# Kernel tuning notes

Measured on AMD Instinct MI355X. Metric: run time of the kernel, lower is better.

Reference implementation:

```python
import jax, jax.numpy as jnp
import numpy as np

N, E, H, NH = 10000, 160000, 128, 8
HD = H // NH
LDIM = 8  # (lmax+1)**2 - 1 with lmax=2
CUTOFF = 5.0


def setup_inputs() -> dict:
    key = jax.random.key(0)
    ks = jax.random.split(key, 20)
    w = lambda k, shape: jax.random.normal(k, shape, jnp.float32) * 0.05
    return dict(
        node_feats=jax.random.normal(ks[0], (N, H), jnp.float32),
        edge_feats=jax.random.normal(ks[1], (E, H), jnp.float32),
        vector_feats=jax.random.normal(ks[2], (N, LDIM, H), jnp.float32),
        distances=jax.random.uniform(ks[3], (E,), jnp.float32) * CUTOFF,
        d_ij=jax.random.normal(ks[4], (E, LDIM), jnp.float32),
        senders=jax.random.randint(ks[5], (E,), 0, N),
        receivers=jax.random.randint(ks[6], (E,), 0, N),
        ln_scale=jnp.ones((H,), jnp.float32),
        ln_bias=jnp.zeros((H,), jnp.float32),
        vln_w=jnp.ones((H,), jnp.float32),
        W_vec=w(ks[7], (H, 3 * H)),
        Wq=w(ks[8], (H, H)), bq=jnp.zeros((H,), jnp.float32),
        Wk=w(ks[9], (H, H)), bk=jnp.zeros((H,), jnp.float32),
        Wv=w(ks[10], (H, H)), bv=jnp.zeros((H,), jnp.float32),
        Wdk=w(ks[11], (H, H)), bdk=jnp.zeros((H,), jnp.float32),
        Wdv=w(ks[12], (H, H)), bdv=jnp.zeros((H,), jnp.float32),
        Ws=w(ks[13], (H, 2 * H)), bs=jnp.zeros((2 * H,), jnp.float32),
        Wo=w(ks[14], (H, 3 * H)), bo=jnp.zeros((3 * H,), jnp.float32),
        Wf=w(ks[15], (H, H)), bf=jnp.zeros((H,), jnp.float32),
        Wsrc=w(ks[16], (H, H)),
        Wtrg=w(ks[17], (H, H)),
    )


def _reject(vec, d):
    # vector rejection of vec [E, L, H] against direction d [E, L]
    proj = (vec * d[:, :, None]).sum(axis=1, keepdims=True)
    return vec - proj * d[:, :, None]


def _forward(node_feats, edge_feats, vector_feats, distances, d_ij, senders, receivers,
             ln_scale, ln_bias, vln_w, W_vec, Wq, bq, Wk, bk, Wv, bv, Wdk, bdk, Wdv, bdv,
             Ws, bs, Wo, bo, Wf, bf, Wsrc, Wtrg):
    silu = jax.nn.silu
    n = node_feats.shape[0]
    # LayerNorm (eps=1e-5) on node feats
    mu = node_feats.mean(-1, keepdims=True)
    xc = node_feats - mu
    var = (xc * xc).mean(-1, keepdims=True)
    x = xc * jax.lax.rsqrt(var + 1e-5) * ln_scale + ln_bias
    # VecLayerNorm with norm_type='none' -> identity norm + learned per-channel scale
    vec = vector_feats * vln_w
    q = (x @ Wq + bq).reshape(-1, NH, HD)
    k = (x @ Wk + bk).reshape(-1, NH, HD)
    v = (x @ Wv + bv).reshape(-1, NH, HD)
    dk = silu(edge_feats @ Wdk + bdk).reshape(-1, NH, HD)
    dv = silu(edge_feats @ Wdv + bdv).reshape(-1, NH, HD)
    vec1, vec2, vec3 = jnp.split(vec @ W_vec, [H, 2 * H], axis=-1)
    vec_dot = (vec1 * vec2).sum(axis=1)  # [N, H]
    # per-edge gathers
    q_i = q[receivers]
    k_j = k[senders]
    v_j = v[senders]
    vec_j = vec[senders]  # [E, LDIM, H]
    # attention-style message with cosine cutoff
    cut = 0.5 * (jnp.cos(distances * (jnp.pi / CUTOFF)) + 1.0) * (distances < CUTOFF)
    attn = silu((q_i * k_j * dk).sum(-1)) * cut[:, None]  # [E, NH]
    vj = ((v_j * dv) * attn[:, :, None]).reshape(-1, H)   # [E, H]
    s1, s2 = jnp.split(silu(vj @ Ws + bs), [H], axis=1)
    vec_msg = vec_j * s1[:, None, :] + s2[:, None, :] * d_ij[:, :, None]
    # scatter reduce to nodes
    node_agg = jax.ops.segment_sum(vj, receivers, num_segments=n)
    vec_agg = jax.ops.segment_sum(vec_msg, receivers, num_segments=n)
    o1, o2, o3 = jnp.split(node_agg @ Wo + bo, [H, 2 * H], axis=1)
    dx = vec_dot * o2 + o3
    dvec = vec3 * o1[:, None, :] + vec_agg
    # edge update (last_layer=False)
    w1 = _reject(vec[receivers] @ Wtrg, d_ij)
    w2 = _reject(vec_j @ Wsrc, -d_ij)
    w_dot = (w1 * w2).sum(axis=1)  # [E, H]
    df_ij = silu(edge_feats @ Wf + bf) * w_dot
    return dx, df_ij, dvec


def reference(node_feats, edge_feats, vector_feats, distances, d_ij, senders, receivers,
              ln_scale, ln_bias, vln_w, W_vec, Wq, bq, Wk, bk, Wv, bv, Wdk, bdk, Wdv, bdv,
              Ws, bs, Wo, bo, Wf, bf, Wsrc, Wtrg):
    return _forward(node_feats, edge_feats, vector_feats, distances, d_ij, senders, receivers,
                    ln_scale, ln_bias, vln_w, W_vec, Wq, bq, Wk, bk, Wv, bv, Wdk, bdk, Wdv, bdv,
                    Ws, bs, Wo, bo, Wf, bf, Wsrc, Wtrg)
```

## Files before the change

kernel.cpp:

```cpp
#include <hip/hip_runtime.h>
#include <math.h>

#define NN 10000
#define NE 160000
#define H  128
#define LD 8

typedef unsigned short ushort_t;
typedef short bf16x8 __attribute__((ext_vector_type(8)));
typedef float f32x4 __attribute__((ext_vector_type(4)));

__device__ __forceinline__ float silu_f(float x){ return x / (1.0f + expf(-x)); }
__device__ __forceinline__ float4 f4z(){ return make_float4(0.f,0.f,0.f,0.f); }

__device__ __forceinline__ ushort_t f2bf(float f){
    union { float f; unsigned int u; } x; x.f = f;
    unsigned int r = x.u + 0x7FFFu + ((x.u >> 16) & 1u);
    return (ushort_t)(r >> 16);
}
__device__ __forceinline__ unsigned int pack2bf(float a, float b){
    return (unsigned int)f2bf(a) | ((unsigned int)f2bf(b) << 16);
}
__device__ __forceinline__ float bf2f_hi(unsigned int u){
    union { unsigned int u; float f; } x; x.u = u & 0xffff0000u; return x.f;
}
__device__ __forceinline__ float bf2f_lo(unsigned int u){
    union { unsigned int u; float f; } x; x.u = u << 16; return x.f;
}
__device__ __forceinline__ float bfu2f(ushort_t u){
    union { unsigned int u; float f; } x; x.u = ((unsigned int)u) << 16; return x.f;
}

__global__ void k_prepw(const float* __restrict__ Wq, const float* __restrict__ Wk,
                        const float* __restrict__ Wv, const float* __restrict__ W_vec,
                        const float* __restrict__ Wtrg, const float* __restrict__ Wsrc,
                        const float* __restrict__ Wdk, const float* __restrict__ Wdv,
                        const float* __restrict__ Ws,  const float* __restrict__ Wf,
                        ushort_t* __restrict__ wqkvT, ushort_t* __restrict__ wvecT,
                        ushort_t* __restrict__ wdkT, ushort_t* __restrict__ wdvT,
                        ushort_t* __restrict__ wsT,
                        ushort_t* __restrict__ wfT_hi, ushort_t* __restrict__ wfT_lo){
    int i = blockIdx.x * 256 + threadIdx.x;
    int n = i >> 7, kk = i & 127;
    if (n < 384){
        float v;
        if (n < 128)      v = Wq[kk*128 + n];
        else if (n < 256) v = Wk[kk*128 + (n-128)];
        else              v = Wv[kk*128 + (n-256)];
        wqkvT[n*128 + kk] = f2bf(v);
    } else if (n < 1024){
        int m = n - 384;
        float v;
        if (m < 384)      v = W_vec[kk*384 + m];
        else if (m < 512) v = Wtrg[kk*128 + (m-384)];
        else              v = Wsrc[kk*128 + (m-512)];
        wvecT[m*128 + kk] = f2bf(v);
    } else if (n < 1152){
        int m = n - 1024;
        wdkT[m*128 + kk] = f2bf(Wdk[kk*128 + m]);
    } else if (n < 1280){
        int m = n - 1152;
        wdvT[m*128 + kk] = f2bf(Wdv[kk*128 + m]);
    } else if (n < 1536){
        int m = n - 1280;
        wsT[m*128 + kk] = f2bf(Ws[kk*256 + m]);
    } else if (n < 1664){
        int m = n - 1536;
        float v = Wf[kk*128 + m];
        ushort_t hi = f2bf(v);
        wfT_hi[m*128 + kk] = hi;
        wfT_lo[m*128 + kk] = f2bf(v - bfu2f(hi));
    }
}

__global__ void k_hist(const int* __restrict__ rcv, int* __restrict__ cnt){
    int e = blockIdx.x * 256 + threadIdx.x;
    if (e < NE) atomicAdd(&cnt[rcv[e]], 1);
}

__global__ __launch_bounds__(256) void k_scan(const int* __restrict__ cnt, int* __restrict__ offs){
    __shared__ int part[256];
    const int t = threadIdx.x;
    const int CH = 40;
    int loc[CH];
    int base = t * CH;
    int lsum = 0;
    if (base < NN){
        #pragma unroll
        for (int i = 0; i < CH; i++){ loc[i] = cnt[base + i]; lsum += loc[i]; }
    }
    part[t] = lsum;
    __syncthreads();
    for (int off = 1; off < 256; off <<= 1){
        int v = (t >= off) ? part[t - off] : 0;
        __syncthreads();
        part[t] += v;
        __syncthreads();
    }
    int ex = part[t] - lsum;
    if (base < NN){
        int run = ex;
        #pragma unroll
        for (int i = 0; i < CH; i++){ offs[base + i] = run; run += loc[i]; }
    }
    if (t == 255) offs[NN] = part[255];
}

__global__ void k_scatter(const int* __restrict__ rcv, const int* __restrict__ offs,
                          int* __restrict__ cnt2, int* __restrict__ eidx){
    int e = blockIdx.x * 256 + threadIdx.x;
    if (e < NE){
        int r = rcv[e];
        int p = atomicAdd(&cnt2[r], 1);
        eidx[offs[r] + p] = e;
    }
}

__global__ __launch_bounds__(256) void k_perm(
    const float* __restrict__ ef, const int* __restrict__ eidx,
    const int* __restrict__ snd, const int* __restrict__ rcv,
    const float* __restrict__ dist, const float* __restrict__ dij,
    float* __restrict__ ef_srt, ushort_t* __restrict__ ef_bf_srt,
    int* __restrict__ snd_srt, int* __restrict__ rcv_srt,
    float* __restrict__ dist_srt, float* __restrict__ dij_srt)
{
    __shared__ int eidx_s[64];
    const int tid = threadIdx.x;
    const int p0  = blockIdx.x * 64;
    if (tid < 64){
        int p = p0 + tid;
        int e = eidx[p];
        eidx_s[tid] = e;
        snd_srt[p]  = snd[e];
        rcv_srt[p]  = rcv[e];
        dist_srt[p] = dist[e];
    }
    __syncthreads();
    const int r = tid >> 2, cq = tid & 3;
    const int e = eidx_s[r];
    const int p = p0 + r;
    const float4* src = (const float4*)(ef + (size_t)e*H + cq*32);
    float4* dst  = (float4*)(ef_srt + (size_t)p*H + cq*32);
    ushort_t* db = ef_bf_srt + (size_t)p*H + cq*32;
    #pragma unroll
    for (int j = 0; j < 8; j++){
        float4 v = src[j];
        dst[j] = v;
        uint2 u; u.x = pack2bf(v.x, v.y); u.y = pack2bf(v.z, v.w);
        *(uint2*)(db + j*4) = u;
    }
    if (cq == 0){
        *(float4*)(dij_srt + (size_t)p*LD)     = *(const float4*)(dij + (size_t)e*LD);
        *(float4*)(dij_srt + (size_t)p*LD + 4) = *(const float4*)(dij + (size_t)e*LD + 4);
    }
}

__global__ __launch_bounds__(128) void node_ln(
    const float* __restrict__ nf, const float* __restrict__ vf,
    const float* __restrict__ ln_s, const float* __restrict__ ln_b,
    const float* __restrict__ vlnw,
    ushort_t* __restrict__ x_bf, ushort_t* __restrict__ vec_bf,
    ushort_t* __restrict__ vec_t)
{
    const int n = blockIdx.x, h = threadIdx.x;
    __shared__ float red[4];
    float xv = nf[(size_t)n*H + h];
    float s1 = xv, s2 = xv*xv;
    #pragma unroll
    for (int o = 32; o >= 1; o >>= 1){
        s1 += __shfl_xor(s1, o, 64);
        s2 += __shfl_xor(s2, o, 64);
    }
    const int wid = h >> 6;
    if ((h & 63) == 0){ red[wid] = s1; red[2+wid] = s2; }
    __syncthreads();
    float mean = (red[0] + red[1]) * (1.0f/H);
    float var  = (red[2] + red[3]) * (1.0f/H) - mean*mean;
    float x = (xv - mean) * rsqrtf(var + 1e-5f) * ln_s[h] + ln_b[h];
    x_bf[(size_t)n*H + h] = f2bf(x);
    float w = vlnw[h];
    union { ushort_t s[8]; uint4 u; } pk;
    #pragma unroll
    for (int l = 0; l < LD; l++){
        size_t i = ((size_t)n*LD + l)*H + h;
        ushort_t b = f2bf(vf[i] * w);
        vec_bf[i] = b;
        pk.s[l] = b;
    }
    *(uint4*)&vec_t[((size_t)n*H + h)*8] = pk.u;
}

__global__ __launch_bounds__(256) void node_qkv(
    const ushort_t* __restrict__ x_bf, const ushort_t* __restrict__ wqkvT,
    const float* __restrict__ bq, const float* __restrict__ bk, const float* __restrict__ bv,
    float* __restrict__ q, ushort_t* __restrict__ k_bf, ushort_t* __restrict__ v_bf)
{
    const int tid  = threadIdx.x;
    const int lane = tid & 63;
    const int m0   = (tid >> 6) * 16;
    const int e0   = blockIdx.x * 64;

    const int mrow = lane & 15;
    const int kblk = lane >> 4;

    f32x4 acc[24];
    #pragma unroll
    for (int nt = 0; nt < 24; nt++) acc[nt] = (f32x4)(0.f);

    int arow = e0 + m0 + mrow; if (arow >= NN) arow = NN-1;
    const ushort_t* Arow = x_bf + (size_t)arow*H + kblk*8;
    const ushort_t* wb   = wqkvT + (size_t)mrow*H + kblk*8;

    #pragma unroll
    for (int ks = 0; ks < 4; ks++){
        bf16x8 a = *(const bf16x8*)(Arow + ks*32);
        #pragma unroll
        for (int nt = 0; nt < 24; nt++){
            bf16x8 b8 = *(const bf16x8*)(wb + (size_t)nt*16*H + ks*32);
            acc[nt] = __builtin_amdgcn_mfma_f32_16x16x32_bf16(a, b8, acc[nt], 0, 0, 0);
        }
    }
    #pragma unroll
    for (int t = 0; t < 8; t++){
        int col = t*16 + mrow;
        float bb = bq[col];
        #pragma unroll
        for (int r = 0; r < 4; r++){
            int row = e0 + m0 + kblk*4 + r;
            if (row < NN) q[(size_t)row*H + col] = acc[t][r] + bb;
        }
    }
    #pragma unroll
    for (int t = 0; t < 8; t++){
        int col = t*16 + mrow;
        float bb = bk[col];
        #pragma unroll
        for (int r = 0; r < 4; r++){
            int row = e0 + m0 + kblk*4 + r;
            if (row < NN) k_bf[(size_t)row*H + col] = f2bf(acc[8+t][r] + bb);
        }
    }
    #pragma unroll
    for (int t = 0; t < 8; t++){
        int col = t*16 + mrow;
        float bb = bv[col];
        #pragma unroll
        for (int r = 0; r < 4; r++){
            int row = e0 + m0 + kblk*4 + r;
            if (row < NN) v_bf[(size_t)row*H + col] = f2bf(acc[16+t][r] + bb);
        }
    }
}

__global__ __launch_bounds__(256) void node_vec(
    const ushort_t* __restrict__ vec_bf, const ushort_t* __restrict__ wvecT,
    float* __restrict__ vdot, ushort_t* __restrict__ vec3,
    ushort_t* __restrict__ Vt_t, ushort_t* __restrict__ Vs_t)
{
    __shared__ ushort_t st_s[64][136];

    const int tid  = threadIdx.x;
    const int lane = tid & 63;
    const int wv   = tid >> 6;
    const int m0   = wv * 16;
    const size_t r0 = (size_t)blockIdx.x * 64;

    const int mrow = lane & 15;
    const int kblk = lane >> 4;

    f32x4 acc[40];
    #pragma unroll
    for (int nt = 0; nt < 40; nt++) acc[nt] = (f32x4)(0.f);

    const ushort_t* Arow = vec_bf + (r0 + m0 + mrow)*H + kblk*8;
    const ushort_t* wb   = wvecT + (size_t)mrow*H + kblk*8;

    #pragma unroll
    for (int ks = 0; ks < 4; ks++){
        bf16x8 a = *(const bf16x8*)(Arow + ks*32);
        #pragma unroll
        for (int nt = 0; nt < 40; nt++){
            bf16x8 b8 = *(const bf16x8*)(wb + (size_t)nt*16*H + ks*32);
            acc[nt] = __builtin_amdgcn_mfma_f32_16x16x32_bf16(a, b8, acc[nt], 0, 0, 0);
        }
    }

    #pragma unroll
    for (int t = 0; t < 8; t++){
        float p = acc[t][0]*acc[t+8][0] + acc[t][1]*acc[t+8][1]
                + acc[t][2]*acc[t+8][2] + acc[t][3]*acc[t+8][3];
        p += __shfl_xor(p, 16, 64);
        if ((kblk & 1) == 0){
            int node = (int)(r0 >> 3) + wv*2 + (kblk >> 1);
            vdot[(size_t)node*H + t*16 + mrow] = p;
        }
    }

    __syncthreads();
    #pragma unroll
    for (int t = 0; t < 8; t++){
        int coln = t*16 + mrow;
        int lr = m0 + kblk*4;
        st_s[lr+0][coln] = f2bf(acc[16+t][0]);
        st_s[lr+1][coln] = f2bf(acc[16+t][1]);
        st_s[lr+2][coln] = f2bf(acc[16+t][2]);
        st_s[lr+3][coln] = f2bf(acc[16+t][3]);
    }
    __syncthreads();
    {
        const int rr = tid >> 2, qq = tid & 3;
        uint4* dst = (uint4*)&vec3[(r0 + rr)*H + qq*32];
        const uint4* src = (const uint4*)&st_s[rr][qq*32];
        dst[0] = src[0]; dst[1] = src[1]; dst[2] = src[2]; dst[3] = src[3];
    }

    #pragma unroll
    for (int g = 0; g < 2; g++){
        __syncthreads();
        const int base = 24 + g*8;
        #pragma unroll
        for (int t = 0; t < 8; t++){
            int coln = t*16 + mrow;
            int lr = m0 + kblk*4;
            st_s[lr+0][coln] = f2bf(acc[base+t][0]);
            st_s[lr+1][coln] = f2bf(acc[base+t][1]);
            st_s[lr+2][coln] = f2bf(acc[base+t][2]);
            st_s[lr+3][coln] = f2bf(acc[base+t][3]);
        }
        __syncthreads();
        ushort_t* dstb = (g == 0) ? Vt_t : Vs_t;
        #pragma unroll
        for (int j = 0; j < 4; j++){
            int p = tid + 256*j;
            int nl = p >> 7, hh = p & 127;
            union { ushort_t s[8]; uint4 u; } pk;
            #pragma unroll
            for (int l = 0; l < 8; l++) pk.s[l] = st_s[nl*8 + l][hh];
            *(uint4*)&dstb[(((r0 >> 3) + nl)*(size_t)H + hh)*8] = pk.u;
        }
    }
}

__global__ __launch_bounds__(256) void edge_attn(
    const ushort_t* __restrict__ ef_bf,
    const ushort_t* __restrict__ wdkT, const float* __restrict__ bdk,
    const ushort_t* __restrict__ wdvT, const float* __restrict__ bdv,
    const int* __restrict__ snd_srt, const int* __restrict__ rcv_srt,
    const float* __restrict__ dist_srt,
    const float* __restrict__ q, const ushort_t* __restrict__ k_bf,
    const ushort_t* __restrict__ v_bf,
    ushort_t* __restrict__ vj)
{
    __shared__ ushort_t dk_s[64][136];
    __shared__ ushort_t dv_s[64][136];

    const int tid  = threadIdx.x;
    const int lane = tid & 63;
    const int m0   = (tid >> 6) * 16;
    const size_t e0 = (size_t)blockIdx.x * 64;

    const int mrow = lane & 15;
    const int kblk = lane >> 4;

    f32x4 accK[8], accV[8];
    #pragma unroll
    for (int nt = 0; nt < 8; nt++){ accK[nt] = (f32x4)(0.f); accV[nt] = (f32x4)(0.f); }

    const ushort_t* Arow = ef_bf + (e0 + m0 + mrow)*H + kblk*8;
    const ushort_t* wkb  = wdkT + (size_t)mrow*H + kblk*8;
    const ushort_t* wvb  = wdvT + (size_t)mrow*H + kblk*8;

    #pragma unroll
    for (int ks = 0; ks < 4; ks++){
        bf16x8 a = *(const bf16x8*)(Arow + ks*32);
        #pragma unroll
        for (int nt = 0; nt < 8; nt++){
            bf16x8 bk8 = *(const bf16x8*)(wkb + (size_t)nt*16*H + ks*32);
            accK[nt] = __builtin_amdgcn_mfma_f32_16x16x32_bf16(a, bk8, accK[nt], 0, 0, 0);
            bf16x8 bv8 = *(const bf16x8*)(wvb + (size_t)nt*16*H + ks*32);
            accV[nt] = __builtin_amdgcn_mfma_f32_16x16x32_bf16(a, bv8, accV[nt], 0, 0, 0);
        }
    }

    const int lrow = m0 + 4*kblk;
    #pragma unroll
    for (int nt = 0; nt < 8; nt++){
        int coln = nt*16 + mrow;
        float bkn = bdk[coln], bvn = bdv[coln];
        #pragma unroll
        for (int r = 0; r < 4; r++){
            dk_s[lrow + r][coln] = f2bf(silu_f(accK[nt][r] + bkn));
            dv_s[lrow + r][coln] = f2bf(silu_f(accV[nt][r] + bvn));
        }
    }
    __syncthreads();

    const int r  = tid >> 2, cq = tid & 3;
    const size_t e = e0 + r;
    const int s  = snd_srt[e], rr = rcv_srt[e];
    const float d = dist_srt[e];
    const float cut = (d < 5.0f) ? 0.5f*(cosf(d*0.6283185307179586f) + 1.0f) : 0.0f;
    const float*    qrow = q    + (size_t)rr*H + cq*32;
    const ushort_t* krow = k_bf + (size_t)s*H + cq*32;
    const ushort_t* vrow = v_bf + (size_t)s*H + cq*32;
    ushort_t* vjrow = vj + e*H + cq*32;

    #pragma unroll
    for (int hh = 0; hh < 2; hh++){
        const int c0 = hh*16;
        float p = 0.f;
        #pragma unroll
        for (int j = 0; j < 4; j++){
            float4 q4 = *(const float4*)(qrow + c0 + 4*j);
            uint2 ku = *(const uint2*)(krow + c0 + 4*j);
            uint2 du = *(const uint2*)&dk_s[r][cq*32 + c0 + 4*j];
            p += q4.x*bf2f_lo(ku.x)*bf2f_lo(du.x) + q4.y*bf2f_hi(ku.x)*bf2f_hi(du.x)
               + q4.z*bf2f_lo(ku.y)*bf2f_lo(du.y) + q4.w*bf2f_hi(ku.y)*bf2f_hi(du.y);
        }
        float attn = silu_f(p) * cut;
        #pragma unroll
        for (int j = 0; j < 4; j++){
            uint2 vu = *(const uint2*)(vrow + c0 + 4*j);
            uint2 du = *(const uint2*)&dv_s[r][cq*32 + c0 + 4*j];
            uint2 u;
            u.x = pack2bf(bf2f_lo(vu.x)*bf2f_lo(du.x)*attn,
                          bf2f_hi(vu.x)*bf2f_hi(du.x)*attn);
            u.y = pack2bf(bf2f_lo(vu.y)*bf2f_lo(du.y)*attn,
                          bf2f_hi(vu.y)*bf2f_hi(du.y)*attn);
            *(uint2*)(vjrow + c0 + 4*j) = u;
        }
    }
}

__global__ __launch_bounds__(256) void edge_s(
    const ushort_t* __restrict__ vj, const ushort_t* __restrict__ wsT,
    const float* __restrict__ bs, unsigned int* __restrict__ s12p)
{
    __shared__ ushort_t s_s[64][264];

    const int tid  = threadIdx.x;
    const int lane = tid & 63;
    const int m0   = (tid >> 6) * 16;
    const size_t e0 = (size_t)blockIdx.x * 64;

    const int mrow = lane & 15;
    const int kblk = lane >> 4;

    f32x4 acc[16];
    #pragma unroll
    for (int nt = 0; nt < 16; nt++) acc[nt] = (f32x4)(0.f);

    const ushort_t* Arow = vj + (e0 + m0 + mrow)*H + kblk*8;
    const ushort_t* wb   = wsT + (size_t)mrow*H + kblk*8;

    #pragma unroll
    for (int ks = 0; ks < 4; ks++){
        bf16x8 a = *(const bf16x8*)(Arow + ks*32);
        #pragma unroll
        for (int nt = 0; nt < 16; nt++){
            bf16x8 b8 = *(const bf16x8*)(wb + (size_t)nt*16*H + ks*32);
            acc[nt] = __builtin_amdgcn_mfma_f32_16x16x32_bf16(a, b8, acc[nt], 0, 0, 0);
        }
    }

    const int lrow = m0 + 4*kblk;
    #pragma unroll
    for (int nt = 0; nt < 16; nt++){
        int coln = nt*16 + mrow;
        float bb = bs[coln];
        #pragma unroll
        for (int r = 0; r < 4; r++)
            s_s[lrow + r][coln] = f2bf(silu_f(acc[nt][r] + bb));
    }
    __syncthreads();

    const int r = tid >> 2, cq = tid & 3;
    #pragma unroll
    for (int j = 0; j < 8; j++){
        int hh = cq*32 + j*4;
        uint4 o;
        o.x = (unsigned)s_s[r][hh+0] | ((unsigned)s_s[r][128+hh+0] << 16);
        o.y = (unsigned)s_s[r][hh+1] | ((unsigned)s_s[r][128+hh+1] << 16);
        o.z = (unsigned)s_s[r][hh+2] | ((unsigned)s_s[r][128+hh+2] << 16);
        o.w = (unsigned)s_s[r][hh+3] | ((unsigned)s_s[r][128+hh+3] << 16);
        *(uint4*)&s12p[(e0 + r)*H + hh] = o;
    }
}

__global__ __launch_bounds__(256) void edge_f(
    const float* __restrict__ ef,
    const ushort_t* __restrict__ wfT_hi, const ushort_t* __restrict__ wfT_lo,
    const float* __restrict__ bf_, float* __restrict__ f)
{
    const int tid  = threadIdx.x;
    const int lane = tid & 63;
    const int m0   = (tid >> 6) * 16;
    const size_t e0 = (size_t)blockIdx.x * 64;

    const int mrow = lane & 15;
    const int kblk = lane >> 4;

    f32x4 acc[8];
    #pragma unroll
    for (int nt = 0; nt < 8; nt++) acc[nt] = (f32x4)(0.f);

    const float* Arow = ef + (e0 + m0 + mrow)*H + kblk*8;
    const ushort_t* wh = wfT_hi + (size_t)mrow*H + kblk*8;
    const ushort_t* wl = wfT_lo + (size_t)mrow*H + kblk*8;

    #pragma unroll
    for (int ks = 0; ks < 4; ks++){
        float4 v0 = *(const float4*)(Arow + ks*32);
        float4 v1 = *(const float4*)(Arow + ks*32 + 4);
        float vv[8] = {v0.x, v0.y, v0.z, v0.w, v1.x, v1.y, v1.z, v1.w};
        union { short s[8]; bf16x8 v; } ah, al;
        #pragma unroll
        for (int j = 0; j < 8; j++){
            ushort_t hi = f2bf(vv[j]);
            ah.s[j] = (short)hi;
            al.s[j] = (short)f2bf(vv[j] - bfu2f(hi));
        }
        #pragma unroll
        for (int nt = 0; nt < 8; nt++){
            bf16x8 bh = *(const bf16x8*)(wh + (size_t)nt*16*H + ks*32);
            bf16x8 bl = *(const bf16x8*)(wl + (size_t)nt*16*H + ks*32);
            acc[nt] = __builtin_amdgcn_mfma_f32_16x16x32_bf16(ah.v, bh, acc[nt], 0, 0, 0);
            acc[nt] = __builtin_amdgcn_mfma_f32_16x16x32_bf16(al.v, bh, acc[nt], 0, 0, 0);
            acc[nt] = __builtin_amdgcn_mfma_f32_16x16x32_bf16(ah.v, bl, acc[nt], 0, 0, 0);
            acc[nt] = __builtin_amdgcn_mfma_f32_16x16x32_bf16(al.v, bl, acc[nt], 0, 0, 0);
        }
    }

    #pragma unroll
    for (int nt = 0; nt < 8; nt++){
        int col = nt*16 + mrow;
        float bb = bf_[col];
        #pragma unroll
        for (int r = 0; r < 4; r++)
            f[(e0 + m0 + 4*kblk + r)*H + col] = silu_f(acc[nt][r] + bb);
    }
}

struct Pref {
    int   s, eo;
    float vjv;
    unsigned p12;
    uint4 uv, ub;
    float4 d0, d1;
    float fv;
};

__global__ __launch_bounds__(512) void node_fuse(
    const int* __restrict__ offs, const int* __restrict__ eidx,
    const int* __restrict__ snd_srt,
    const ushort_t* __restrict__ vj, const unsigned int* __restrict__ s12p,
    const float* __restrict__ dij_srt, const ushort_t* __restrict__ vec_t,
    const float* __restrict__ f,
    const ushort_t* __restrict__ Vt_t, const ushort_t* __restrict__ Vs_t,
    const float* __restrict__ Wo, const float* __restrict__ bo,
    const float* __restrict__ vdot, const ushort_t* __restrict__ vec3,
    float* __restrict__ dx, float* __restrict__ df, float* __restrict__ dvec)
{
    const int n = blockIdx.x;
    const int tid = threadIdx.x;
    const int h = tid & 127;
    const int par = tid >> 7;
    const int beg = offs[n], end = offs[n+1];

    float AT[LD];
    {
        uint4 ut = *(const uint4*)&Vt_t[((size_t)n*H + h)*8];
        AT[0]=bf2f_lo(ut.x); AT[1]=bf2f_hi(ut.x);
        AT[2]=bf2f_lo(ut.y); AT[3]=bf2f_hi(ut.y);
        AT[4]=bf2f_lo(ut.z); AT[5]=bf2f_hi(ut.z);
        AT[6]=bf2f_lo(ut.w); AT[7]=bf2f_hi(ut.w);
    }

    float na = 0.f;
    float av[LD];
    #pragma unroll
    for (int l = 0; l < LD; l++) av[l] = 0.f;

    Pref cur, nxt;
    int i = beg + par;
    if (i < end){
        int s = snd_srt[i];
        cur.s   = s;
        cur.eo  = eidx[i];
        cur.vjv = bfu2f(vj[(size_t)i*H + h]);
        cur.p12 = s12p[(size_t)i*H + h];
        cur.uv  = *(const uint4*)&vec_t[((size_t)s*H + h)*8];
        cur.ub  = *(const uint4*)&Vs_t[((size_t)s*H + h)*8];
        cur.d0  = *(const float4*)&dij_srt[(size_t)i*LD];
        cur.d1  = *(const float4*)&dij_srt[(size_t)i*LD + 4];
        cur.fv  = f[(size_t)i*H + h];
    }

    while (i < end){
        const int j = i + 4;
        if (j < end){
            int s = snd_srt[j];
            nxt.s   = s;
            nxt.eo  = eidx[j];
            nxt.vjv = bfu2f(vj[(size_t)j*H + h]);
            nxt.p12 = s12p[(size_t)j*H + h];
            nxt.uv  = *(const uint4*)&vec_t[((size_t)s*H + h)*8];
            nxt.ub  = *(const uint4*)&Vs_t[((size_t)s*H + h)*8];
            nxt.d0  = *(const float4*)&dij_srt[(size_t)j*LD];
            nxt.d1  = *(const float4*)&dij_srt[(size_t)j*LD + 4];
            nxt.fv  = f[(size_t)j*H + h];
        }

        float s1 = bf2f_lo(cur.p12), s2 = bf2f_hi(cur.p12);
        na += cur.vjv;
        float dl[LD];
        dl[0]=cur.d0.x; dl[1]=cur.d0.y; dl[2]=cur.d0.z; dl[3]=cur.d0.w;
        dl[4]=cur.d1.x; dl[5]=cur.d1.y; dl[6]=cur.d1.z; dl[7]=cur.d1.w;
        float dd = 0.f;
        #pragma unroll
        for (int l = 0; l < LD; l++) dd = fmaf(dl[l], dl[l], dd);
        const float c2 = 2.0f - dd;

        float vvx[LD], Blx[LD];
        vvx[0]=bf2f_lo(cur.uv.x); vvx[1]=bf2f_hi(cur.uv.x);
        vvx[2]=bf2f_lo(cur.uv.y); vvx[3]=bf2f_hi(cur.uv.y);
        vvx[4]=bf2f_lo(cur.uv.z); vvx[5]=bf2f_hi(cur.uv.z);
        vvx[6]=bf2f_lo(cur.uv.w); vvx[7]=bf2f_hi(cur.uv.w);
        Blx[0]=bf2f_lo(cur.ub.x); Blx[1]=bf2f_hi(cur.ub.x);
        Blx[2]=bf2f_lo(cur.ub.y); Blx[3]=bf2f_hi(cur.ub.y);
        Blx[4]=bf2f_lo(cur.ub.z); Blx[5]=bf2f_hi(cur.ub.z);
        Blx[6]=bf2f_lo(cur.ub.w); Blx[7]=bf2f_hi(cur.ub.w);

        float AB = 0.f, aa_ = 0.f, bb_ = 0.f;
        #pragma unroll
        for (int l = 0; l < LD; l++){
            av[l] = fmaf(vvx[l], s1, fmaf(dl[l], s2, av[l]));
            AB  = fmaf(AT[l], Blx[l], AB);
            aa_ = fmaf(AT[l], dl[l], aa_);
            bb_ = fmaf(Blx[l], dl[l], bb_);
        }
        df[(size_t)cur.eo*H + h] = cur.fv * (AB - aa_*bb_*c2);

        cur = nxt;
        i = j;
    }

    __shared__ float pl[4][LD+1][128];
    __shared__ float o_s[3][128];
    #pragma unroll
    for (int l = 0; l < LD; l++) pl[par][l][h] = av[l];
    pl[par][LD][h] = na;
    __syncthreads();

    if (par == 0){
        #pragma unroll
        for (int l = 0; l <= LD; l++)
            pl[0][l][h] = (pl[0][l][h] + pl[1][l][h]) + (pl[2][l][h] + pl[3][l][h]);
    }
    __syncthreads();

    if (par > 0){
        const int g = par - 1;
        float o = bo[g*H + h];
        for (int kk = 0; kk < H; kk++)
            o = fmaf(pl[0][LD][kk], Wo[kk*(3*H) + g*H + h], o);
        o_s[g][h] = o;
    }
    __syncthreads();

    if (par == 0){
        dx[(size_t)n*H + h] = fmaf(vdot[(size_t)n*H + h], o_s[1][h], o_s[2][h]);
        #pragma unroll
        for (int l = 0; l < LD; l++){
            size_t i2 = ((size_t)n*LD + l)*H + h;
            dvec[i2] = fmaf(bfu2f(vec3[i2]), o_s[0][h], pl[0][l][h]);
        }
    }
}

extern "C" void kernel_launch(void* const* d_in, const int* in_sizes, int n_in,
                              void* d_out, int out_size, void* d_ws, size_t ws_size,
                              hipStream_t stream) {
    const float* nf    = (const float*)d_in[0];
    const float* ef    = (const float*)d_in[1];
    const float* vf    = (const float*)d_in[2];
    const float* dist  = (const float*)d_in[3];
    const float* dij   = (const float*)d_in[4];
    const int*   snd   = (const int*)d_in[5];
    const int*   rcv   = (const int*)d_in[6];
    const float* ln_s  = (const float*)d_in[7];
    const float* ln_b  = (const float*)d_in[8];
    const float* vlnw  = (const float*)d_in[9];
    const float* W_vec = (const float*)d_in[10];
    const float* Wq    = (const float*)d_in[11];
    const float* bq    = (const float*)d_in[12];
    const float* Wk    = (const float*)d_in[13];
    const float* bk    = (const float*)d_in[14];
    const float* Wv    = (const float*)d_in[15];
    const float* bv    = (const float*)d_in[16];
    const float* Wdk   = (const float*)d_in[17];
    const float* bdk   = (const float*)d_in[18];
    const float* Wdv   = (const float*)d_in[19];
    const float* bdv   = (const float*)d_in[20];
    const float* Ws    = (const float*)d_in[21];
    const float* bs    = (const float*)d_in[22];
    const float* Wo    = (const float*)d_in[23];
    const float* bo    = (const float*)d_in[24];
    const float* Wf    = (const float*)d_in[25];
    const float* bf_   = (const float*)d_in[26];
    const float* Wsrc  = (const float*)d_in[27];
    const float* Wtrg  = (const float*)d_in[28];

    float* out  = (float*)d_out;
    float* dx   = out;
    float* df   = out + (size_t)NN*H;
    float* dvec = df + (size_t)NE*H;

    float* w = (float*)d_ws;
    size_t off = 0;
    float* q    = w + off; off += (size_t)NN*H;
    float* vdot = w + off; off += (size_t)NN*H;
    ushort_t* k_bf   = (ushort_t*)(w + off); off += (size_t)NN*H/2;
    ushort_t* v_bf   = (ushort_t*)(w + off); off += (size_t)NN*H/2;
    ushort_t* x_bf   = (ushort_t*)(w + off); off += (size_t)NN*H/2;
    ushort_t* vec_bf = (ushort_t*)(w + off); off += (size_t)NN*LD*H/2;
    ushort_t* vec_t  = (ushort_t*)(w + off); off += (size_t)NN*LD*H/2;
    ushort_t* vec3   = (ushort_t*)(w + off); off += (size_t)NN*LD*H/2;
    ushort_t* Vt_t   = (ushort_t*)(w + off); off += (size_t)NN*LD*H/2;
    ushort_t* Vs_t   = (ushort_t*)(w + off); off += (size_t)NN*LD*H/2;
    ushort_t* vj     = (ushort_t*)(w + off); off += (size_t)NE*H/2;
    float*        ef_srt = (float*)(w + off);
    unsigned int* s12p   = (unsigned int*)(w + off); off += (size_t)NE*H;
    ushort_t* ef_bf_srt = (ushort_t*)(w + off);
    float*    f         = (float*)(w + off); off += (size_t)NE*H;
    ushort_t* wqkvT  = (ushort_t*)(w + off); off += 384*128/2;
    ushort_t* wvecT  = (ushort_t*)(w + off); off += 640*128/2;
    ushort_t* wdkT   = (ushort_t*)(w + off); off += 128*128/2;
    ushort_t* wdvT   = (ushort_t*)(w + off); off += 128*128/2;
    ushort_t* wsT    = (ushort_t*)(w + off); off += 256*128/2;
    ushort_t* wfT_hi = (ushort_t*)(w + off); off += 128*128/2;
    ushort_t* wfT_lo = (ushort_t*)(w + off); off += 128*128/2;
    int* cnt  = (int*)(w + off); off += NN;
    int* cnt2 = (int*)(w + off); off += NN;
    int* offs = (int*)(w + off); off += NN + 1;
    int* eidx = (int*)(w + off); off += NE;
    int* snd_srt = (int*)(w + off); off += NE;
    int* rcv_srt = (int*)(w + off); off += NE;
    float* dist_srt = (float*)(w + off); off += NE;
    float* dij_srt  = (float*)(w + off); off += (size_t)NE*LD;

    hipMemsetAsync(cnt,  0, NN*sizeof(int), stream);
    hipMemsetAsync(cnt2, 0, NN*sizeof(int), stream);

    k_prepw<<<832, 256, 0, stream>>>(Wq, Wk, Wv, W_vec, Wtrg, Wsrc, Wdk, Wdv, Ws, Wf,
                                     wqkvT, wvecT, wdkT, wdvT, wsT, wfT_hi, wfT_lo);

    k_hist<<<(NE+255)/256, 256, 0, stream>>>(rcv, cnt);
    k_scan<<<1, 256, 0, stream>>>(cnt, offs);
    k_scatter<<<(NE+255)/256, 256, 0, stream>>>(rcv, offs, cnt2, eidx);

    k_perm<<<NE/64, 256, 0, stream>>>(ef, eidx, snd, rcv, dist, dij,
                                      ef_srt, ef_bf_srt, snd_srt, rcv_srt,
                                      dist_srt, dij_srt);

    node_ln<<<NN, 128, 0, stream>>>(nf, vf, ln_s, ln_b, vlnw, x_bf, vec_bf, vec_t);

    node_qkv<<<(NN+63)/64, 256, 0, stream>>>(x_bf, wqkvT, bq, bk, bv, q, k_bf, v_bf);

    node_vec<<<NN*LD/64, 256, 0, stream>>>(vec_bf, wvecT, vdot, vec3, Vt_t, Vs_t);

    edge_attn<<<NE/64, 256, 0, stream>>>(ef_bf_srt, wdkT, bdk, wdvT, bdv,
                                         snd_srt, rcv_srt, dist_srt, q, k_bf, v_bf, vj);

    edge_f<<<NE/64, 256, 0, stream>>>(ef_srt, wfT_hi, wfT_lo, bf_, f);

    edge_s<<<NE/64, 256, 0, stream>>>(vj, wsT, bs, s12p);

    node_fuse<<<NN, 512, 0, stream>>>(offs, eidx, snd_srt, vj, s12p, dij_srt, vec_t,
                                      f, Vt_t, Vs_t, Wo, bo, vdot, vec3, dx, df, dvec);
}
```

Measured before the change: 883.3 us.

## Fuse edge attention, Wf and Ws GEMMs into one edge kernel with bf16 intermediates

Merges edge_attn, edge_f and edge_s into a single per-64-edge kernel. vj is kept in shared memory for the Ws GEMM rather than re-read from global. k_perm now writes precomputed hi/lo bf16 splits of the edge features instead of an fp32 copy plus a bf16 copy, and the silu(ef@Wf) result is stored as bf16 in place over the lo buffer rather than as fp32. This cuts global traffic and launch count, at the cost of higher register and shared-memory pressure per block and reduced precision of f in the df output.

New measurement: 893.0 us. Within noise of the previous version (+1.1%).

```diff
diff --git a/kernel.cpp b/kernel.cpp
--- a/kernel.cpp
+++ b/kernel.cpp
@@ -11,7 +11,6 @@
 typedef float f32x4 __attribute__((ext_vector_type(4)));
 
 __device__ __forceinline__ float silu_f(float x){ return x / (1.0f + expf(-x)); }
-__device__ __forceinline__ float4 f4z(){ return make_float4(0.f,0.f,0.f,0.f); }
 
 __device__ __forceinline__ ushort_t f2bf(float f){
     union { float f; unsigned int u; } x; x.f = f;
@@ -120,7 +119,7 @@
     const float* __restrict__ ef, const int* __restrict__ eidx,
     const int* __restrict__ snd, const int* __restrict__ rcv,
     const float* __restrict__ dist, const float* __restrict__ dij,
-    float* __restrict__ ef_srt, ushort_t* __restrict__ ef_bf_srt,
+    ushort_t* __restrict__ ef_hi, ushort_t* __restrict__ ef_lo,
     int* __restrict__ snd_srt, int* __restrict__ rcv_srt,
     float* __restrict__ dist_srt, float* __restrict__ dij_srt)
 {
@@ -140,14 +139,19 @@
     const int e = eidx_s[r];
     const int p = p0 + r;
     const float4* src = (const float4*)(ef + (size_t)e*H + cq*32);
-    float4* dst  = (float4*)(ef_srt + (size_t)p*H + cq*32);
-    ushort_t* db = ef_bf_srt + (size_t)p*H + cq*32;
+    ushort_t* dh = ef_hi + (size_t)p*H + cq*32;
+    ushort_t* dl = ef_lo + (size_t)p*H + cq*32;
     #pragma unroll
     for (int j = 0; j < 8; j++){
         float4 v = src[j];
-        dst[j] = v;
-        uint2 u; u.x = pack2bf(v.x, v.y); u.y = pack2bf(v.z, v.w);
-        *(uint2*)(db + j*4) = u;
+        ushort_t hx = f2bf(v.x), hy = f2bf(v.y), hz = f2bf(v.z), hw = f2bf(v.w);
+        ushort_t lx = f2bf(v.x - bfu2f(hx)), ly = f2bf(v.y - bfu2f(hy));
+        ushort_t lz = f2bf(v.z - bfu2f(hz)), lw = f2bf(v.w - bfu2f(hw));
+        uint2 uh, ul;
+        uh.x = (unsigned)hx | ((unsigned)hy << 16); uh.y = (unsigned)hz | ((unsigned)hw << 16);
+        ul.x = (unsigned)lx | ((unsigned)ly << 16); ul.y = (unsigned)lz | ((unsigned)lw << 16);
+        *(uint2*)(dh + j*4) = uh;
+        *(uint2*)(dl + j*4) = ul;
     }
     if (cq == 0){
         *(float4*)(dij_srt + (size_t)p*LD)     = *(const float4*)(dij + (size_t)e*LD);
@@ -341,203 +345,176 @@
     }
 }
 
-__global__ __launch_bounds__(256) void edge_attn(
-    const ushort_t* __restrict__ ef_bf,
+__global__ __launch_bounds__(256) void edge_mega(
+    const ushort_t* __restrict__ ef_hi, ushort_t* __restrict__ ef_lo_f,
     const ushort_t* __restrict__ wdkT, const float* __restrict__ bdk,
     const ushort_t* __restrict__ wdvT, const float* __restrict__ bdv,
+    const ushort_t* __restrict__ wfT_hi, const ushort_t* __restrict__ wfT_lo,
+    const float* __restrict__ bf_,
+    const ushort_t* __restrict__ wsT, const float* __restrict__ bs,
     const int* __restrict__ snd_srt, const int* __restrict__ rcv_srt,
     const float* __restrict__ dist_srt,
     const float* __restrict__ q, const ushort_t* __restrict__ k_bf,
     const ushort_t* __restrict__ v_bf,
-    ushort_t* __restrict__ vj)
+    ushort_t* __restrict__ vj, unsigned int* __restrict__ s12p)
 {
-    __shared__ ushort_t dk_s[64][136];
-    __shared__ ushort_t dv_s[64][136];
+    __shared__ union {
+        struct { ushort_t dk[64][136]; ushort_t dv[64][136]; } a;
+        ushort_t s_s[64][264];
+    } U;
+    __shared__ ushort_t vj_s[64][136];
 
     const int tid  = threadIdx.x;
     const int lane = tid & 63;
     const int m0   = (tid >> 6) * 16;
     const size_t e0 = (size_t)blockIdx.x * 64;
-
     const int mrow = lane & 15;
     const int kblk = lane >> 4;
 
-    f32x4 accK[8], accV[8];
-    #pragma unroll
-    for (int nt = 0; nt < 8; nt++){ accK[nt] = (f32x4)(0.f); accV[nt] = (f32x4)(0.f); }
-
-    const ushort_t* Arow = ef_bf + (e0 + m0 + mrow)*H + kblk*8;
-    const ushort_t* wkb  = wdkT + (size_t)mrow*H + kblk*8;
-    const ushort_t* wvb  = wdvT + (size_t)mrow*H + kblk*8;
-
-    #pragma unroll
-    for (int ks = 0; ks < 4; ks++){
-        bf16x8 a = *(const bf16x8*)(Arow + ks*32);
+    {
+        f32x4 accK[8], accV[8];
+        #pragma unroll
+        for (int nt = 0; nt < 8; nt++){ accK[nt] = (f32x4)(0.f); accV[nt] = (f32x4)(0.f); }
+        const ushort_t* Arow = ef_hi + (e0 + m0 + mrow)*H + kblk*8;
+        const ushort_t* wkb  = wdkT + (size_t)mrow*H + kblk*8;
+        const ushort_t* wvb  = wdvT + (size_t)mrow*H + kblk*8;
+        #pragma unroll
+        for (int ks = 0; ks < 4; ks++){
+            bf16x8 a = *(const bf16x8*)(Arow + ks*32);
+            #pragma unroll
+            for (int nt = 0; nt < 8; nt++){
+                bf16x8 bk8 = *(const bf16x8*)(wkb + (size_t)nt*16*H + ks*32);
+                accK[nt] = __builtin_amdgcn_mfma_f32_16x16x32_bf16(a, bk8, accK[nt], 0, 0, 0);
+                bf16x8 bv8 = *(const bf16x8*)(wvb + (size_t)nt*16*H + ks*32);
+                accV[nt] = __builtin_amdgcn_mfma_f32_16x16x32_bf16(a, bv8, accV[nt], 0, 0, 0);
+            }
+        }
+        const int lrow = m0 + 4*kblk;
         #pragma unroll
         for (int nt = 0; nt < 8; nt++){
-            bf16x8 bk8 = *(const bf16x8*)(wkb + (size_t)nt*16*H + ks*32);
-            accK[nt] = __builtin_amdgcn_mfma_f32_16x16x32_bf16(a, bk8, accK[nt], 0, 0, 0);
-            bf16x8 bv8 = *(const bf16x8*)(wvb + (size_t)nt*16*H + ks*32);
-            accV[nt] = __builtin_amdgcn_mfma_f32_16x16x32_bf16(a, bv8, accV[nt], 0, 0, 0);
-        }
-    }
-
-    const int lrow = m0 + 4*kblk;
-    #pragma unroll
-    for (int nt = 0; nt < 8; nt++){
-        int coln = nt*16 + mrow;
-        float bkn = bdk[coln], bvn = bdv[coln];
-        #pragma unroll
-        for (int r = 0; r < 4; r++){
-            dk_s[lrow + r][coln] = f2bf(silu_f(accK[nt][r] + bkn));
-            dv_s[lrow + r][coln] = f2bf(silu_f(accV[nt][r] + bvn));
-        }
-    }
-    __syncthreads();
-
-    const int r  = tid >> 2, cq = tid & 3;
-    const size_t e = e0 + r;
-    const int s  = snd_srt[e], rr = rcv_srt[e];
-    const float d = dist_srt[e];
-    const float cut = (d < 5.0f) ? 0.5f*(cosf(d*0.6283185307179586f) + 1.0f) : 0.0f;
-    const float*    qrow = q    + (size_t)rr*H + cq*32;
-    const ushort_t* krow = k_bf + (size_t)s*H + cq*32;
-    const ushort_t* vrow = v_bf + (size_t)s*H + cq*32;
-    ushort_t* vjrow = vj + e*H + cq*32;
-
-    #pragma unroll
-    for (int hh = 0; hh < 2; hh++){
-        const int c0 = hh*16;
-        float p = 0.f;
-        #pragma unroll
-        for (int j = 0; j < 4; j++){
-            float4 q4 = *(const float4*)(qrow + c0 + 4*j);
-            uint2 ku = *(const uint2*)(krow + c0 + 4*j);
-            uint2 du = *(const uint2*)&dk_s[r][cq*32 + c0 + 4*j];
-            p += q4.x*bf2f_lo(ku.x)*bf2f_lo(du.x) + q4.y*bf2f_hi(ku.x)*bf2f_hi(du.x)
-               + q4.z*bf2f_lo(ku.y)*bf2f_lo(du.y) + q4.w*bf2f_hi(ku.y)*bf2f_hi(du.y);
-        }
-        float attn = silu_f(p) * cut;
-        #pragma unroll
-        for (int j = 0; j < 4; j++){
-            uint2 vu = *(const uint2*)(vrow + c0 + 4*j);
-            uint2 du = *(const uint2*)&dv_s[r][cq*32 + c0 + 4*j];
-            uint2 u;
-            u.x = pack2bf(bf2f_lo(vu.x)*bf2f_lo(du.x)*attn,
-                          bf2f_hi(vu.x)*bf2f_hi(du.x)*attn);
-            u.y = pack2bf(bf2f_lo(vu.y)*bf2f_lo(du.y)*attn,
-                          bf2f_hi(vu.y)*bf2f_hi(du.y)*attn);
-            *(uint2*)(vjrow + c0 + 4*j) = u;
-        }
-    }
-}
-
-__global__ __launch_bounds__(256) void edge_s(
-    const ushort_t* __restrict__ vj, const ushort_t* __restrict__ wsT,
-    const float* __restrict__ bs, unsigned int* __restrict__ s12p)
-{
-    __shared__ ushort_t s_s[64][264];
-
-    const int tid  = threadIdx.x;
-    const int lane = tid & 63;
-    const int m0   = (tid >> 6) * 16;
-    const size_t e0 = (size_t)blockIdx.x * 64;
-
-    const int mrow = lane & 15;
-    const int kblk = lane >> 4;
-
-    f32x4 acc[16];
-    #pragma unroll
-    for (int nt = 0; nt < 16; nt++) acc[nt] = (f32x4)(0.f);
-
-    const ushort_t* Arow = vj + (e0 + m0 + mrow)*H + kblk*8;
-    const ushort_t* wb   = wsT + (size_t)mrow*H + kblk*8;
-
-    #pragma unroll
-    for (int ks = 0; ks < 4; ks++){
-        bf16x8 a = *(const bf16x8*)(Arow + ks*32);
+            int coln = nt*16 + mrow;
+            float bkn = bdk[coln], bvn = bdv[coln];
+            #pragma unroll
+            for (int r = 0; r < 4; r++){
+                U.a.dk[lrow + r][coln] = f2bf(silu_f(accK[nt][r] + bkn));
+                U.a.dv[lrow + r][coln] = f2bf(silu_f(accV[nt][r] + bvn));
+            }
+        }
+    }
+    __syncthreads();
+
+    {
+        const int r  = tid >> 2, cq = tid & 3;
+        const size_t e = e0 + r;
+        const int s  = snd_srt[e], rr = rcv_srt[e];
+        const float d = dist_srt[e];
+        const float cut = (d < 5.0f) ? 0.5f*(cosf(d*0.6283185307179586f) + 1.0f) : 0.0f;
+        const float*    qrow = q    + (size_t)rr*H + cq*32;
+        const ushort_t* krow = k_bf + (size_t)s*H + cq*32;
+        const ushort_t* vrow = v_bf + (size_t)s*H + cq*32;
+        ushort_t* vjrow = vj + e*H + cq*32;
+
+        #pragma unroll
+        for (int hh = 0; hh < 2; hh++){
+            const int c0 = hh*16;
+            float p = 0.f;
+            #pragma unroll
+            for (int j = 0; j < 4; j++){
+                float4 q4 = *(const float4*)(qrow + c0 + 4*j);
+                uint2 ku = *(const uint2*)(krow + c0 + 4*j);
+                uint2 du = *(const uint2*)&U.a.dk[r][cq*32 + c0 + 4*j];
+                p += q4.x*bf2f_lo(ku.x)*bf2f_lo(du.x) + q4.y*bf2f_hi(ku.x)*bf2f_hi(du.x)
+                   + q4.z*bf2f_lo(ku.y)*bf2f_lo(du.y) + q4.w*bf2f_hi(ku.y)*bf2f_hi(du.y);
+            }
+            float attn = silu_f(p) * cut;
+            #pragma unroll
+            for (int j = 0; j < 4; j++){
+                uint2 vu = *(const uint2*)(vrow + c0 + 4*j);
+                uint2 du = *(const uint2*)&U.a.dv[r][cq*32 + c0 + 4*j];
+                uint2 u;
+                u.x = pack2bf(bf2f_lo(vu.x)*bf2f_lo(du.x)*attn,
+                              bf2f_hi(vu.x)*bf2f_hi(du.x)*attn);
+                u.y = pack2bf(bf2f_lo(vu.y)*bf2f_lo(du.y)*attn,
+                              bf2f_hi(vu.y)*bf2f_hi(du.y)*attn);
+                *(uint2*)(vjrow + c0 + 4*j) = u;
+                *(uint2*)&vj_s[r][cq*32 + c0 + 4*j] = u;
+            }
+        }
+    }
+    __syncthreads();
+
+    {
+        f32x4 accF[8];
+        #pragma unroll
+        for (int nt = 0; nt < 8; nt++) accF[nt] = (f32x4)(0.f);
+        const ushort_t* Ah = ef_hi   + (e0 + m0 + mrow)*H + kblk*8;
+        const ushort_t* Al = ef_lo_f + (e0 + m0 + mrow)*H + kblk*8;
+        const ushort_t* wh = wfT_hi + (size_t)mrow*H + kblk*8;
+        const ushort_t* wl = wfT_lo + (size_t)mrow*H + kblk*8;
+        #pragma unroll
+        for (int ks = 0; ks < 4; ks++){
+            bf16x8 ah = *(const bf16x8*)(Ah + ks*32);
+            bf16x8 al = *(const bf16x8*)(Al + ks*32);
+            #pragma unroll
+            for (int nt = 0; nt < 8; nt++){
+                bf16x8 bh = *(const bf16x8*)(wh + (size_t)nt*16*H + ks*32);
+                bf16x8 bl = *(const bf16x8*)(wl + (size_t)nt*16*H + ks*32);
+                accF[nt] = __builtin_amdgcn_mfma_f32_16x16x32_bf16(ah, bh, accF[nt], 0, 0, 0);
+                accF[nt] = __builtin_amdgcn_mfma_f32_16x16x32_bf16(al, bh, accF[nt], 0, 0, 0);
+                accF[nt] = __builtin_amdgcn_mfma_f32_16x16x32_bf16(ah, bl, accF[nt], 0, 0, 0);
+                accF[nt] = __builtin_amdgcn_mfma_f32_16x16x32_bf16(al, bl, accF[nt], 0, 0, 0);
+            }
+        }
+        __syncthreads();
+        #pragma unroll
+        for (int nt = 0; nt < 8; nt++){
+            int col = nt*16 + mrow;
+            float bb = bf_[col];
+            #pragma unroll
+            for (int r = 0; r < 4; r++)
+                ef_lo_f[(e0 + m0 + 4*kblk + r)*H + col] = f2bf(silu_f(accF[nt][r] + bb));
+        }
+    }
+
+    {
+        f32x4 accS[16];
+        #pragma unroll
+        for (int nt = 0; nt < 16; nt++) accS[nt] = (f32x4)(0.f);
+        const ushort_t* ArowL = &vj_s[m0 + mrow][kblk*8];
+        const ushort_t* wb    = wsT + (size_t)mrow*H + kblk*8;
+        #pragma unroll
+        for (int ks = 0; ks < 4; ks++){
+            bf16x8 a = *(const bf16x8*)(ArowL + ks*32);
+            #pragma unroll
+            for (int nt = 0; nt < 16; nt++){
+                bf16x8 b8 = *(const bf16x8*)(wb + (size_t)nt*16*H + ks*32);
+                accS[nt] = __builtin_amdgcn_mfma_f32_16x16x32_bf16(a, b8, accS[nt], 0, 0, 0);
+            }
+        }
+        const int lrow = m0 + 4*kblk;
         #pragma unroll
         for (int nt = 0; nt < 16; nt++){
-            bf16x8 b8 = *(const bf16x8*)(wb + (size_t)nt*16*H + ks*32);
-            acc[nt] = __builtin_amdgcn_mfma_f32_16x16x32_bf16(a, b8, acc[nt], 0, 0, 0);
-        }
-    }
-
-    const int lrow = m0 + 4*kblk;
-    #pragma unroll
-    for (int nt = 0; nt < 16; nt++){
-        int coln = nt*16 + mrow;
-        float bb = bs[coln];
-        #pragma unroll
-        for (int r = 0; r < 4; r++)
-            s_s[lrow + r][coln] = f2bf(silu_f(acc[nt][r] + bb));
-    }
-    __syncthreads();
-
-    const int r = tid >> 2, cq = tid & 3;
-    #pragma unroll
-    for (int j = 0; j < 8; j++){
-        int hh = cq*32 + j*4;
-        uint4 o;
-        o.x = (unsigned)s_s[r][hh+0] | ((unsigned)s_s[r][128+hh+0] << 16);
-        o.y = (unsigned)s_s[r][hh+1] | ((unsigned)s_s[r][128+hh+1] << 16);
-        o.z = (unsigned)s_s[r][hh+2] | ((unsigned)s_s[r][128+hh+2] << 16);
-        o.w = (unsigned)s_s[r][hh+3] | ((unsigned)s_s[r][128+hh+3] << 16);
-        *(uint4*)&s12p[(e0 + r)*H + hh] = o;
-    }
-}
-
-__global__ __launch_bounds__(256) void edge_f(
-    const float* __restrict__ ef,
-    const ushort_t* __restrict__ wfT_hi, const ushort_t* __restrict__ wfT_lo,
-    const float* __restrict__ bf_, float* __restrict__ f)
-{
-    const int tid  = threadIdx.x;
-    const int lane = tid & 63;
-    const int m0   = (tid >> 6) * 16;
-    const size_t e0 = (size_t)blockIdx.x * 64;
-
-    const int mrow = lane & 15;
-    const int kblk = lane >> 4;
-
-    f32x4 acc[8];
-    #pragma unroll
-    for (int nt = 0; nt < 8; nt++) acc[nt] = (f32x4)(0.f);
-
-    const float* Arow = ef + (e0 + m0 + mrow)*H + kblk*8;
-    const ushort_t* wh = wfT_hi + (size_t)mrow*H + kblk*8;
-    const ushort_t* wl = wfT_lo + (size_t)mrow*H + kblk*8;
-
-    #pragma unroll
-    for (int ks = 0; ks < 4; ks++){
-        float4 v0 = *(const float4*)(Arow + ks*32);
-        float4 v1 = *(const float4*)(Arow + ks*32 + 4);
-        float vv[8] = {v0.x, v0.y, v0.z, v0.w, v1.x, v1.y, v1.z, v1.w};
-        union { short s[8]; bf16x8 v; } ah, al;
+            int coln = nt*16 + mrow;
+            float bb = bs[coln];
+            #pragma unroll
+            for (int r = 0; r < 4; r++)
+                U.s_s[lrow + r][coln] = f2bf(silu_f(accS[nt][r] + bb));
+        }
+    }
+    __syncthreads();
+
+    {
+        const int r = tid >> 2, cq = tid & 3;
         #pragma unroll
         for (int j = 0; j < 8; j++){
-            ushort_t hi = f2bf(vv[j]);
-            ah.s[j] = (short)hi;
-            al.s[j] = (short)f2bf(vv[j] - bfu2f(hi));
-        }
-        #pragma unroll
-        for (int nt = 0; nt < 8; nt++){
-            bf16x8 bh = *(const bf16x8*)(wh + (size_t)nt*16*H + ks*32);
-            bf16x8 bl = *(const bf16x8*)(wl + (size_t)nt*16*H + ks*32);
-            acc[nt] = __builtin_amdgcn_mfma_f32_16x16x32_bf16(ah.v, bh, acc[nt], 0, 0, 0);
-            acc[nt] = __builtin_amdgcn_mfma_f32_16x16x32_bf16(al.v, bh, acc[nt], 0, 0, 0);
-            acc[nt] = __builtin_amdgcn_mfma_f32_16x16x32_bf16(ah.v, bl, acc[nt], 0, 0, 0);
-            acc[nt] = __builtin_amdgcn_mfma_f32_16x16x32_bf16(al.v, bl, acc[nt], 0, 0, 0);
-        }
-    }
-
-    #pragma unroll
-    for (int nt = 0; nt < 8; nt++){
-        int col = nt*16 + mrow;
-        float bb = bf_[col];
-        #pragma unroll
-        for (int r = 0; r < 4; r++)
-            f[(e0 + m0 + 4*kblk + r)*H + col] = silu_f(acc[nt][r] + bb);
+            int hh = cq*32 + j*4;
+            uint4 o;
+            o.x = (unsigned)U.s_s[r][hh+0] | ((unsigned)U.s_s[r][128+hh+0] << 16);
+            o.y = (unsigned)U.s_s[r][hh+1] | ((unsigned)U.s_s[r][128+hh+1] << 16);
+            o.z = (unsigned)U.s_s[r][hh+2] | ((unsigned)U.s_s[r][128+hh+2] << 16);
+            o.w = (unsigned)U.s_s[r][hh+3] | ((unsigned)U.s_s[r][128+hh+3] << 16);
+            *(uint4*)&s12p[(e0 + r)*H + hh] = o;
+        }
     }
 }
 
@@ -555,7 +532,7 @@
     const int* __restrict__ snd_srt,
     const ushort_t* __restrict__ vj, const unsigned int* __restrict__ s12p,
     const float* __restrict__ dij_srt, const ushort_t* __restrict__ vec_t,
-    const float* __restrict__ f,
+    const ushort_t* __restrict__ f_bf,
     const ushort_t* __restrict__ Vt_t, const ushort_t* __restrict__ Vs_t,
     const float* __restrict__ Wo, const float* __restrict__ bo,
     const float* __restrict__ vdot, const ushort_t* __restrict__ vec3,
@@ -593,7 +570,7 @@
         cur.ub  = *(const uint4*)&Vs_t[((size_t)s*H + h)*8];
         cur.d0  = *(const float4*)&dij_srt[(size_t)i*LD];
         cur.d1  = *(const float4*)&dij_srt[(size_t)i*LD + 4];
-        cur.fv  = f[(size_t)i*H + h];
+        cur.fv  = bfu2f(f_bf[(size_t)i*H + h]);
     }
 
     while (i < end){
@@ -608,7 +585,7 @@
             nxt.ub  = *(const uint4*)&Vs_t[((size_t)s*H + h)*8];
             nxt.d0  = *(const float4*)&dij_srt[(size_t)j*LD];
             nxt.d1  = *(const float4*)&dij_srt[(size_t)j*LD + 4];
-            nxt.fv  = f[(size_t)j*H + h];
+            nxt.fv  = bfu2f(f_bf[(size_t)j*H + h]);
         }
 
         float s1 = bf2f_lo(cur.p12), s2 = bf2f_hi(cur.p12);
@@ -729,10 +706,10 @@
     ushort_t* Vt_t   = (ushort_t*)(w + off); off += (size_t)NN*LD*H/2;
     ushort_t* Vs_t   = (ushort_t*)(w + off); off += (size_t)NN*LD*H/2;
     ushort_t* vj     = (ushort_t*)(w + off); off += (size_t)NE*H/2;
-    float*        ef_srt = (float*)(w + off);
-    unsigned int* s12p   = (unsigned int*)(w + off); off += (size_t)NE*H;
-    ushort_t* ef_bf_srt = (ushort_t*)(w + off);
-    float*    f         = (float*)(w + off); off += (size_t)NE*H;
+    ushort_t* ef_hi  = (ushort_t*)(w + off); off += (size_t)NE*H/2;
+    ushort_t* ef_lo  = (ushort_t*)(w + off); off += (size_t)NE*H/2;
+    ushort_t* f_bf   = ef_lo;
+    unsigned int* s12p = (unsigned int*)(w + off); off += (size_t)NE*H;
     ushort_t* wqkvT  = (ushort_t*)(w + off); off += 384*128/2;
     ushort_t* wvecT  = (ushort_t*)(w + off); off += 640*128/2;
     ushort_t* wdkT   = (ushort_t*)(w + off); off += 128*128/2;
@@ -760,7 +737,7 @@
     k_scatter<<<(NE+255)/256, 256, 0, stream>>>(rcv, offs, cnt2, eidx);
 
     k_perm<<<NE/64, 256, 0, stream>>>(ef, eidx, snd, rcv, dist, dij,
-                                      ef_srt, ef_bf_srt, snd_srt, rcv_srt,
+                                      ef_hi, ef_lo, snd_srt, rcv_srt,
                                       dist_srt, dij_srt);
 
     node_ln<<<NN, 128, 0, stream>>>(nf, vf, ln_s, ln_b, vlnw, x_bf, vec_bf, vec_t);
@@ -769,13 +746,12 @@
 
     node_vec<<<NN*LD/64, 256, 0, stream>>>(vec_bf, wvecT, vdot, vec3, Vt_t, Vs_t);
 
-    edge_attn<<<NE/64, 256, 0, stream>>>(ef_bf_srt, wdkT, bdk, wdvT, bdv,
-                                         snd_srt, rcv_srt, dist_srt, q, k_bf, v_bf, vj);
-
-    edge_f<<<NE/64, 256, 0, stream>>>(ef_srt, wfT_hi, wfT_lo, bf_, f);
-
-    edge_s<<<NE/64, 256, 0, stream>>>(vj, wsT, bs, s12p);
+    edge_mega<<<NE/64, 256, 0, stream>>>(ef_hi, ef_lo, wdkT, bdk, wdvT, bdv,
+                                         wfT_hi, wfT_lo, bf_, wsT, bs,
+                                         snd_srt, rcv_srt, dist_srt,
+                                         q, k_bf, v_bf, vj, s12p);
 
     node_fuse<<<NN, 512, 0, stream>>>(offs, eidx, snd_srt, vj, s12p, dij_srt, vec_t,
-                                      f, Vt_t, Vs_t, Wo, bo, vdot, vec3, dx, df, dvec);
-}
+                                      f_bf, Vt_t, Vs_t, Wo, bo, vdot, vec3,
+                                      dx, df, dvec);
+}
```
